# Kernel optimization log

Hardware: AMD Instinct MI355X
Metric: run time of the kernel (lower is better)

## Reference

```python
import jax, jax.numpy as jnp
import numpy as np

N_NODES = 100000
EMB_DIM = 64
N_EDGES = 1200000
N_LAYERS = 3


def setup_inputs() -> dict:
    key = jax.random.key(0)
    k1, k2, k3 = jax.random.split(key, 3)
    embedding = jax.random.normal(k1, (N_NODES, EMB_DIM), dtype=jnp.float32)
    layer_weights = jnp.ones((N_LAYERS + 1,), dtype=jnp.float32) / (N_LAYERS + 1)
    edge_weight = jax.random.uniform(k2, (N_EDGES,), dtype=jnp.float32)
    edge_index = jax.random.randint(k3, (2, N_EDGES), 0, N_NODES, dtype=jnp.int64)
    return {"embedding": embedding, "layer_weights": layer_weights,
            "edge_weight": edge_weight, "edge_index": edge_index}


def reference(embedding, layer_weights, edge_weight, edge_index):
    # LightGCN inference (dropout off). Each LGConv applies gcn_norm
    # (no self loops) then scatter-adds norm * x[src] into dst.
    n = embedding.shape[0]
    row, col = edge_index[0], edge_index[1]  # source, target

    # gcn_norm: deg over target nodes, symmetric normalization
    deg = jax.ops.segment_sum(edge_weight, col, num_segments=n)
    dinv = jnp.where(deg > 0, jax.lax.rsqrt(deg), 0.0)
    norm = dinv[row] * edge_weight * dinv[col]  # [E]

    x = embedding
    outs = [x]
    for _ in range(N_LAYERS):
        msgs = norm[:, None] * x[row]                         # [E, D] gather
        x = jax.ops.segment_sum(msgs, col, num_segments=n)    # [N, D] scatter
        outs.append(x)

    w = jax.nn.softmax(layer_weights)                         # [L+1]
    comb = jnp.einsum('l,lnd->nd', w, jnp.stack(outs))        # weighted layer combine
    # F.normalize(dim=1), eps=1e-12
    nrm = jnp.maximum(jnp.linalg.norm(comb, axis=1, keepdims=True), 1e-12)
    return comb / nrm
```

## Files before the change

kernel.cpp:

```cpp
#include <hip/hip_runtime.h>

#define N_NODES 100000
#define EMB_DIM 64
#define N_EDGES 1200000

#define BSHIFT  7
#define BNODES  128
#define NBUCKET ((N_NODES + BNODES - 1) / BNODES)
#define CAP     2048
#define EPB     4096
#define NBLK_BIN ((N_EDGES + EPB - 1) / EPB)

#define DBINS 512
#define DNPB  1024
#define NBLK_DEG ((N_NODES + DNPB - 1) / DNPB)

struct __align__(8) EdgeRec {
    int   s;
    float w;
};

struct __align__(8) BinRec {
    unsigned meta;
    float    ew;
};

__device__ __forceinline__ unsigned short f2bf(float f) {
    unsigned u = __float_as_uint(f);
    u += 0x7FFFu + ((u >> 16) & 1u);
    return (unsigned short)(u >> 16);
}
__device__ __forceinline__ float bf2f(unsigned short h) {
    return __uint_as_float((unsigned)h << 16);
}

__global__ void init_kernel(int* __restrict__ bucket_cursor, int* __restrict__ dhist) {
    int t = threadIdx.x;
    if (t < NBUCKET) bucket_cursor[t] = t * CAP;
    if (t < DBINS)   dhist[t] = 0;
}

__global__ void bin_scatter(const int* __restrict__ row,
                            const int* __restrict__ col,
                            const float* __restrict__ ew,
                            int* __restrict__ bucket_cursor,
                            BinRec* __restrict__ binned) {
    __shared__ int hcnt[NBUCKET];
    __shared__ int hbase[NBUCKET];
    int tid = threadIdx.x;
    if (tid < NBUCKET) hcnt[tid] = 0;
    __syncthreads();
    int base = blockIdx.x * EPB;
    int end = base + EPB; if (end > N_EDGES) end = N_EDGES;
    for (int e = base + tid; e < end; e += 1024)
        atomicAdd(&hcnt[col[e] >> BSHIFT], 1);
    __syncthreads();
    if (tid < NBUCKET) {
        int c = hcnt[tid];
        hbase[tid] = c ? atomicAdd(&bucket_cursor[tid], c) : 0;
        hcnt[tid] = 0;
    }
    __syncthreads();
    for (int e = base + tid; e < end; e += 1024) {
        int c = col[e];
        int b = c >> BSHIFT;
        int rk = atomicAdd(&hcnt[b], 1);
        BinRec r;
        r.meta = (unsigned)row[e] | ((unsigned)(c & (BNODES - 1)) << 20);
        r.ew = ew[e];
        binned[hbase[b] + rk] = r;
    }
}

__global__ void bucket_scan(const int* __restrict__ cursor,
                            int* __restrict__ csr_base,
                            int* __restrict__ start) {
    __shared__ int ws[16];
    int t = threadIdx.x;
    int lane = t & 63, wid = t >> 6;
    int v = (t < NBUCKET) ? (cursor[t] - t * CAP) : 0;
    int inc = v;
    #pragma unroll
    for (int o = 1; o < 64; o <<= 1) {
        int u = __shfl_up(inc, o, 64);
        if (lane >= o) inc += u;
    }
    if (lane == 63) ws[wid] = inc;
    __syncthreads();
    int woff = 0;
    for (int w = 0; w < wid; ++w) woff += ws[w];
    if (t < NBUCKET) csr_base[t] = woff + inc - v;
    if (t == 0) start[N_NODES] = N_EDGES;
}

__global__ void bucket_build(const BinRec* __restrict__ binned,
                             const int* __restrict__ cursor,
                             const int* __restrict__ csr_base,
                             float* __restrict__ dinv,
                             float* __restrict__ rdinv,
                             int* __restrict__ start,
                             EdgeRec* __restrict__ rec) {
    __shared__ int   cnt[BNODES];
    __shared__ float deg[BNODES];
    __shared__ int   cur[BNODES];
    __shared__ int   wsum[2];
    int b = blockIdx.x;
    int tid = threadIdx.x;
    if (tid < BNODES) { cnt[tid] = 0; deg[tid] = 0.0f; }
    __syncthreads();
    int s = b * CAP;
    int n = cursor[b] - s;
    for (int i = tid; i < n; i += 256) {
        BinRec r = binned[s + i];
        int l = r.meta >> 20;
        atomicAdd(&cnt[l], 1);
        atomicAdd(&deg[l], r.ew);
    }
    __syncthreads();
    int lane = tid & 63, wid = tid >> 6;
    int v = (tid < BNODES) ? cnt[tid] : 0;
    int inc = v;
    #pragma unroll
    for (int o = 1; o < 64; o <<= 1) {
        int u = __shfl_up(inc, o, 64);
        if (lane >= o) inc += u;
    }
    if (tid < BNODES && lane == 63) wsum[wid] = inc;
    __syncthreads();
    if (tid < BNODES) {
        int excl = inc - v + ((wid == 1) ? wsum[0] : 0);
        int node = (b << BSHIFT) + tid;
        if (node < N_NODES) {
            int st = csr_base[b] + excl;
            start[node] = st;
            cur[tid] = st;
            float d = deg[tid];
            dinv[node]  = (d > 0.0f) ? rsqrtf(d) : 0.0f;
            rdinv[node] = (d > 0.0f) ? sqrtf(d)  : 0.0f;
        } else {
            cur[tid] = 0;
        }
    }
    __syncthreads();
    for (int i = tid; i < n; i += 256) {
        BinRec r = binned[s + i];
        int l = r.meta >> 20;
        int pos = atomicAdd(&cur[l], 1);
        EdgeRec o;
        o.s = (int)(r.meta & 0xFFFFFu);
        o.w = r.ew;
        rec[pos] = o;
    }
}

__global__ void cvt_y0(const float* __restrict__ emb,
                       const float* __restrict__ dinv,
                       unsigned short* __restrict__ y0) {
    int t = blockIdx.x * blockDim.x + threadIdx.x;
    long base = (long)t * 8;
    if (base + 8 <= (long)N_NODES * EMB_DIM) {
        float dn = dinv[t >> 3];
        float4 a = *(const float4*)(emb + base);
        float4 b = *(const float4*)(emb + base + 4);
        uint4 o;
        o.x = (unsigned)f2bf(dn * a.x) | ((unsigned)f2bf(dn * a.y) << 16);
        o.y = (unsigned)f2bf(dn * a.z) | ((unsigned)f2bf(dn * a.w) << 16);
        o.z = (unsigned)f2bf(dn * b.x) | ((unsigned)f2bf(dn * b.y) << 16);
        o.w = (unsigned)f2bf(dn * b.z) | ((unsigned)f2bf(dn * b.w) << 16);
        *(uint4*)(y0 + base) = o;
    }
}

__global__ void deg_hist(const int* __restrict__ start, int* __restrict__ dhist) {
    __shared__ int h[DBINS];
    int tid = threadIdx.x;
    for (int i = tid; i < DBINS; i += 256) h[i] = 0;
    __syncthreads();
    int base = blockIdx.x * DNPB;
    int end = base + DNPB; if (end > N_NODES) end = N_NODES;
    for (int n = base + tid; n < end; n += 256) {
        int d = start[n + 1] - start[n];
        if (d > DBINS - 1) d = DBINS - 1;
        atomicAdd(&h[d], 1);
    }
    __syncthreads();
    for (int i = tid; i < DBINS; i += 256)
        if (h[i]) atomicAdd(&dhist[i], h[i]);
}

__global__ void deg_scan(const int* __restrict__ dhist, int* __restrict__ dcursor) {
    __shared__ int ws[8];
    int t = threadIdx.x;
    int lane = t & 63, wid = t >> 6;
    int v = dhist[t];
    int inc = v;
    #pragma unroll
    for (int o = 1; o < 64; o <<= 1) {
        int u = __shfl_up(inc, o, 64);
        if (lane >= o) inc += u;
    }
    if (lane == 63) ws[wid] = inc;
    __syncthreads();
    int woff = 0;
    for (int w = 0; w < wid; ++w) woff += ws[w];
    dcursor[t] = woff + inc - v;
}

__global__ void deg_scatter(const int* __restrict__ start,
                            int* __restrict__ dcursor,
                            int* __restrict__ perm) {
    __shared__ int h[DBINS];
    __shared__ int hb[DBINS];
    int tid = threadIdx.x;
    for (int i = tid; i < DBINS; i += 256) h[i] = 0;
    __syncthreads();
    int base = blockIdx.x * DNPB;
    int end = base + DNPB; if (end > N_NODES) end = N_NODES;
    for (int n = base + tid; n < end; n += 256) {
        int d = start[n + 1] - start[n];
        if (d > DBINS - 1) d = DBINS - 1;
        atomicAdd(&h[d], 1);
    }
    __syncthreads();
    for (int i = tid; i < DBINS; i += 256) {
        int c = h[i];
        hb[i] = c ? atomicAdd(&dcursor[i], c) : 0;
        h[i] = 0;
    }
    __syncthreads();
    for (int n = base + tid; n < end; n += 256) {
        int d = start[n + 1] - start[n];
        if (d > DBINS - 1) d = DBINS - 1;
        int rk = atomicAdd(&h[d], 1);
        perm[hb[d] + rk] = n;
    }
}

__global__ void prop16_kernel(const unsigned short* __restrict__ yin,
                              unsigned short* __restrict__ yout,
                              const EdgeRec* __restrict__ rec,
                              const int* __restrict__ start,
                              const float* __restrict__ dinv,
                              const int* __restrict__ perm) {
    int t = blockIdx.x * blockDim.x + threadIdx.x;
    int slot = t >> 4;
    int q = (t & 15) << 2;
    if (slot >= N_NODES) return;
    int n = perm[slot];
    int s = start[n], e = start[n + 1];
    float a0 = 0.f, a1 = 0.f, a2 = 0.f, a3 = 0.f;
    int j = s;
    for (; j + 2 <= e; j += 2) {
        EdgeRec r0 = rec[j], r1 = rec[j + 1];
        ushort4 h0 = *(const ushort4*)(yin + (((size_t)r0.s) << 6) + q);
        ushort4 h1 = *(const ushort4*)(yin + (((size_t)r1.s) << 6) + q);
        a0 += r0.w * bf2f(h0.x) + r1.w * bf2f(h1.x);
        a1 += r0.w * bf2f(h0.y) + r1.w * bf2f(h1.y);
        a2 += r0.w * bf2f(h0.z) + r1.w * bf2f(h1.z);
        a3 += r0.w * bf2f(h0.w) + r1.w * bf2f(h1.w);
    }
    if (j < e) {
        EdgeRec r = rec[j];
        ushort4 h = *(const ushort4*)(yin + (((size_t)r.s) << 6) + q);
        a0 += r.w * bf2f(h.x);
        a1 += r.w * bf2f(h.y);
        a2 += r.w * bf2f(h.z);
        a3 += r.w * bf2f(h.w);
    }
    float dn = dinv[n];
    float dn2 = dn * dn;
    ushort4 o;
    o.x = f2bf(dn2 * a0);
    o.y = f2bf(dn2 * a1);
    o.z = f2bf(dn2 * a2);
    o.w = f2bf(dn2 * a3);
    *(ushort4*)(yout + (((size_t)n) << 6) + q) = o;
}

__global__ void prop16_combine_kernel(const unsigned short* __restrict__ y2h,
                                      const float* __restrict__ x0,
                                      const unsigned short* __restrict__ y1h,
                                      const EdgeRec* __restrict__ rec,
                                      const int* __restrict__ start,
                                      const float* __restrict__ dinv,
                                      const float* __restrict__ rdinv,
                                      const float* __restrict__ lw,
                                      const int* __restrict__ perm,
                                      float* __restrict__ out) {
    int t = blockIdx.x * blockDim.x + threadIdx.x;
    int slot = t >> 4;
    int q = (t & 15) << 2;
    if (slot >= N_NODES) return;
    int n = perm[slot];
    int s = start[n], e = start[n + 1];
    float a0 = 0.f, a1 = 0.f, a2 = 0.f, a3 = 0.f;
    int j = s;
    for (; j + 2 <= e; j += 2) {
        EdgeRec r0 = rec[j], r1 = rec[j + 1];
        ushort4 h0 = *(const ushort4*)(y2h + (((size_t)r0.s) << 6) + q);
        ushort4 h1 = *(const ushort4*)(y2h + (((size_t)r1.s) << 6) + q);
        a0 += r0.w * bf2f(h0.x) + r1.w * bf2f(h1.x);
        a1 += r0.w * bf2f(h0.y) + r1.w * bf2f(h1.y);
        a2 += r0.w * bf2f(h0.z) + r1.w * bf2f(h1.z);
        a3 += r0.w * bf2f(h0.w) + r1.w * bf2f(h1.w);
    }
    if (j < e) {
        EdgeRec r = rec[j];
        ushort4 h = *(const ushort4*)(y2h + (((size_t)r.s) << 6) + q);
        a0 += r.w * bf2f(h.x);
        a1 += r.w * bf2f(h.y);
        a2 += r.w * bf2f(h.z);
        a3 += r.w * bf2f(h.w);
    }
    float dn = dinv[n];
    float rn = rdinv[n];
    float x3v0 = dn * a0, x3v1 = dn * a1, x3v2 = dn * a2, x3v3 = dn * a3;

    float w0 = lw[0], w1 = lw[1], w2 = lw[2], w3 = lw[3];
    float m = fmaxf(fmaxf(w0, w1), fmaxf(w2, w3));
    float e0 = expf(w0 - m), e1 = expf(w1 - m), e2 = expf(w2 - m), e3 = expf(w3 - m);
    float inv_s = 1.0f / (e0 + e1 + e2 + e3);

    size_t off = (((size_t)n) << 6) + q;
    float4 xv = *(const float4*)(x0 + off);
    ushort4 h1v = *(const ushort4*)(y1h + off);
    ushort4 h2v = *(const ushort4*)(y2h + off);

    float v0 = (e0 * xv.x + e1 * bf2f(h1v.x) * rn + e2 * bf2f(h2v.x) * rn + e3 * x3v0) * inv_s;
    float v1 = (e0 * xv.y + e1 * bf2f(h1v.y) * rn + e2 * bf2f(h2v.y) * rn + e3 * x3v1) * inv_s;
    float v2 = (e0 * xv.z + e1 * bf2f(h1v.z) * rn + e2 * bf2f(h2v.z) * rn + e3 * x3v2) * inv_s;
    float v3 = (e0 * xv.w + e1 * bf2f(h1v.w) * rn + e2 * bf2f(h2v.w) * rn + e3 * x3v3) * inv_s;

    float sq = v0 * v0 + v1 * v1 + v2 * v2 + v3 * v3;
    #pragma unroll
    for (int o = 1; o < 16; o <<= 1) sq += __shfl_xor(sq, o, 64);
    float nrm = fmaxf(sqrtf(sq), 1e-12f);
    float inv_n = 1.0f / nrm;

    float4 ov;
    ov.x = v0 * inv_n; ov.y = v1 * inv_n; ov.z = v2 * inv_n; ov.w = v3 * inv_n;
    *(float4*)(out + off) = ov;
}

extern "C" void kernel_launch(void* const* d_in, const int* in_sizes, int n_in,
                              void* d_out, int out_size, void* d_ws, size_t ws_size,
                              hipStream_t stream) {
    const float* emb = (const float*)d_in[0];
    const float* lw  = (const float*)d_in[1];
    const float* ew  = (const float*)d_in[2];
    const int*   ei  = (const int*)d_in[3];
    const int* row = ei;
    const int* col = ei + N_EDGES;
    float* out = (float*)d_out;

    char* p = (char*)d_ws;
    BinRec*  binned = (BinRec*)p;               p += (size_t)NBUCKET * CAP * sizeof(BinRec);
    EdgeRec* rec    = (EdgeRec*)p;              p += (size_t)N_EDGES * sizeof(EdgeRec);
    unsigned short* y0h = (unsigned short*)p;   p += (size_t)N_NODES * EMB_DIM * 2;
    unsigned short* y1h = (unsigned short*)p;   p += (size_t)N_NODES * EMB_DIM * 2;
    unsigned short* y2h = (unsigned short*)p;   p += (size_t)N_NODES * EMB_DIM * 2;
    float* dinv  = (float*)p;                   p += (size_t)N_NODES * 4;
    float* rdinv = (float*)p;                   p += (size_t)N_NODES * 4;
    int*   startA= (int*)p;                     p += (size_t)(N_NODES + 8) * 4;
    int*   perm  = (int*)p;                     p += (size_t)N_NODES * 4;
    int*   csr_base      = (int*)p;             p += (size_t)NBUCKET * 4;
    int*   bucket_cursor = (int*)p;             p += (size_t)NBUCKET * 4;
    int*   dhist   = (int*)p;                   p += (size_t)DBINS * 4;
    int*   dcursor = (int*)p;                   p += (size_t)DBINS * 4;

    const int B = 256;

    init_kernel<<<1, 1024, 0, stream>>>(bucket_cursor, dhist);
    bin_scatter<<<NBLK_BIN, 1024, 0, stream>>>(row, col, ew, bucket_cursor, binned);
    bucket_scan<<<1, 1024, 0, stream>>>(bucket_cursor, csr_base, startA);
    bucket_build<<<NBUCKET, B, 0, stream>>>(binned, bucket_cursor, csr_base,
                                            dinv, rdinv, startA, rec);
    cvt_y0<<<(N_NODES * EMB_DIM / 8 + B - 1) / B, B, 0, stream>>>(emb, dinv, y0h);
    deg_hist<<<NBLK_DEG, B, 0, stream>>>(startA, dhist);
    deg_scan<<<1, DBINS, 0, stream>>>(dhist, dcursor);
    deg_scatter<<<NBLK_DEG, B, 0, stream>>>(startA, dcursor, perm);

    long pt = (long)N_NODES * 16;
    int pgrid = (int)((pt + B - 1) / B);
    prop16_kernel<<<pgrid, B, 0, stream>>>(y0h, y1h, rec, startA, dinv, perm);
    prop16_kernel<<<pgrid, B, 0, stream>>>(y1h, y2h, rec, startA, dinv, perm);
    prop16_combine_kernel<<<pgrid, B, 0, stream>>>(y2h, emb, y1h, rec, startA, dinv,
                                                   rdinv, lw, perm, out);
}
```

Measured before the change: 168.9 us.

## Fuse y0 conversion and degree histogram into bucket_build; widen propagation to 8 lanes per node

Folds the bf16 y0 conversion and the degree histogram into bucket_build, which removes two kernel launches and a reread of start/dinv. The propagation and combine kernels now use 8 threads per node, each loading 16-byte bf16 vectors, with the edge loop unrolled by 4. This gives more memory-level parallelism per thread and fewer threads in total. The cost is higher register pressure and lower occupancy, and the average degree of 12 per node limits how much the 4-way unroll helps.

```diff
diff --git a/kernel.cpp b/kernel.cpp
--- a/kernel.cpp
+++ b/kernel.cpp
@@ -14,6 +14,8 @@
 #define DBINS 512
 #define DNPB  1024
 #define NBLK_DEG ((N_NODES + DNPB - 1) / DNPB)
+
+typedef unsigned short ushort8v __attribute__((ext_vector_type(8)));
 
 struct __align__(8) EdgeRec {
     int   s;
@@ -96,17 +98,22 @@
 __global__ void bucket_build(const BinRec* __restrict__ binned,
                              const int* __restrict__ cursor,
                              const int* __restrict__ csr_base,
+                             const float* __restrict__ emb,
                              float* __restrict__ dinv,
                              float* __restrict__ rdinv,
                              int* __restrict__ start,
-                             EdgeRec* __restrict__ rec) {
+                             EdgeRec* __restrict__ rec,
+                             unsigned short* __restrict__ y0,
+                             int* __restrict__ dhist) {
     __shared__ int   cnt[BNODES];
     __shared__ float deg[BNODES];
     __shared__ int   cur[BNODES];
+    __shared__ int   dh[DBINS];
     __shared__ int   wsum[2];
     int b = blockIdx.x;
     int tid = threadIdx.x;
     if (tid < BNODES) { cnt[tid] = 0; deg[tid] = 0.0f; }
+    for (int i = tid; i < DBINS; i += 256) dh[i] = 0;
     __syncthreads();
     int s = b * CAP;
     int n = cursor[b] - s;
@@ -137,6 +144,8 @@
             float d = deg[tid];
             dinv[node]  = (d > 0.0f) ? rsqrtf(d) : 0.0f;
             rdinv[node] = (d > 0.0f) ? sqrtf(d)  : 0.0f;
+            int dd = v; if (dd > DBINS - 1) dd = DBINS - 1;
+            atomicAdd(&dh[dd], 1);
         } else {
             cur[tid] = 0;
         }
@@ -151,41 +160,27 @@
         o.w = r.ew;
         rec[pos] = o;
     }
-}
-
-__global__ void cvt_y0(const float* __restrict__ emb,
-                       const float* __restrict__ dinv,
-                       unsigned short* __restrict__ y0) {
-    int t = blockIdx.x * blockDim.x + threadIdx.x;
-    long base = (long)t * 8;
-    if (base + 8 <= (long)N_NODES * EMB_DIM) {
-        float dn = dinv[t >> 3];
-        float4 a = *(const float4*)(emb + base);
-        float4 b = *(const float4*)(emb + base + 4);
-        uint4 o;
-        o.x = (unsigned)f2bf(dn * a.x) | ((unsigned)f2bf(dn * a.y) << 16);
-        o.y = (unsigned)f2bf(dn * a.z) | ((unsigned)f2bf(dn * a.w) << 16);
-        o.z = (unsigned)f2bf(dn * b.x) | ((unsigned)f2bf(dn * b.y) << 16);
-        o.w = (unsigned)f2bf(dn * b.z) | ((unsigned)f2bf(dn * b.w) << 16);
-        *(uint4*)(y0 + base) = o;
-    }
-}
-
-__global__ void deg_hist(const int* __restrict__ start, int* __restrict__ dhist) {
-    __shared__ int h[DBINS];
-    int tid = threadIdx.x;
-    for (int i = tid; i < DBINS; i += 256) h[i] = 0;
-    __syncthreads();
-    int base = blockIdx.x * DNPB;
-    int end = base + DNPB; if (end > N_NODES) end = N_NODES;
-    for (int n = base + tid; n < end; n += 256) {
-        int d = start[n + 1] - start[n];
-        if (d > DBINS - 1) d = DBINS - 1;
-        atomicAdd(&h[d], 1);
-    }
-    __syncthreads();
     for (int i = tid; i < DBINS; i += 256)
-        if (h[i]) atomicAdd(&dhist[i], h[i]);
+        if (dh[i]) atomicAdd(&dhist[i], dh[i]);
+    #pragma unroll
+    for (int pass = 0; pass < 4; ++pass) {
+        int g = (pass * 256 + tid) * 8;
+        int l = g >> 6;
+        int node = (b << BSHIFT) + l;
+        if (node < N_NODES) {
+            float d = deg[l];
+            float dn = (d > 0.0f) ? rsqrtf(d) : 0.0f;
+            size_t off = (((size_t)node) << 6) + (g & 63);
+            float4 a = *(const float4*)(emb + off);
+            float4 bb = *(const float4*)(emb + off + 4);
+            uint4 o;
+            o.x = (unsigned)f2bf(dn * a.x)  | ((unsigned)f2bf(dn * a.y)  << 16);
+            o.y = (unsigned)f2bf(dn * a.z)  | ((unsigned)f2bf(dn * a.w)  << 16);
+            o.z = (unsigned)f2bf(dn * bb.x) | ((unsigned)f2bf(dn * bb.y) << 16);
+            o.w = (unsigned)f2bf(dn * bb.z) | ((unsigned)f2bf(dn * bb.w) << 16);
+            *(uint4*)(y0 + off) = o;
+        }
+    }
 }
 
 __global__ void deg_scan(const int* __restrict__ dhist, int* __restrict__ dcursor) {
@@ -236,110 +231,131 @@
     }
 }
 
-__global__ void prop16_kernel(const unsigned short* __restrict__ yin,
-                              unsigned short* __restrict__ yout,
-                              const EdgeRec* __restrict__ rec,
-                              const int* __restrict__ start,
-                              const float* __restrict__ dinv,
-                              const int* __restrict__ perm) {
+__global__ void prop8_kernel(const unsigned short* __restrict__ yin,
+                             unsigned short* __restrict__ yout,
+                             const EdgeRec* __restrict__ rec,
+                             const int* __restrict__ start,
+                             const float* __restrict__ dinv,
+                             const int* __restrict__ perm) {
     int t = blockIdx.x * blockDim.x + threadIdx.x;
-    int slot = t >> 4;
-    int q = (t & 15) << 2;
+    int slot = t >> 3;
+    int q = (t & 7) << 3;
     if (slot >= N_NODES) return;
     int n = perm[slot];
     int s = start[n], e = start[n + 1];
     float a0 = 0.f, a1 = 0.f, a2 = 0.f, a3 = 0.f;
+    float a4 = 0.f, a5 = 0.f, a6 = 0.f, a7 = 0.f;
     int j = s;
-    for (; j + 2 <= e; j += 2) {
-        EdgeRec r0 = rec[j], r1 = rec[j + 1];
-        ushort4 h0 = *(const ushort4*)(yin + (((size_t)r0.s) << 6) + q);
-        ushort4 h1 = *(const ushort4*)(yin + (((size_t)r1.s) << 6) + q);
-        a0 += r0.w * bf2f(h0.x) + r1.w * bf2f(h1.x);
-        a1 += r0.w * bf2f(h0.y) + r1.w * bf2f(h1.y);
-        a2 += r0.w * bf2f(h0.z) + r1.w * bf2f(h1.z);
-        a3 += r0.w * bf2f(h0.w) + r1.w * bf2f(h1.w);
-    }
-    if (j < e) {
+    for (; j + 4 <= e; j += 4) {
+        EdgeRec r0 = rec[j], r1 = rec[j + 1], r2 = rec[j + 2], r3 = rec[j + 3];
+        ushort8v h0 = *(const ushort8v*)(yin + (((size_t)r0.s) << 6) + q);
+        ushort8v h1 = *(const ushort8v*)(yin + (((size_t)r1.s) << 6) + q);
+        ushort8v h2 = *(const ushort8v*)(yin + (((size_t)r2.s) << 6) + q);
+        ushort8v h3 = *(const ushort8v*)(yin + (((size_t)r3.s) << 6) + q);
+        a0 += r0.w * bf2f(h0[0]) + r1.w * bf2f(h1[0]) + r2.w * bf2f(h2[0]) + r3.w * bf2f(h3[0]);
+        a1 += r0.w * bf2f(h0[1]) + r1.w * bf2f(h1[1]) + r2.w * bf2f(h2[1]) + r3.w * bf2f(h3[1]);
+        a2 += r0.w * bf2f(h0[2]) + r1.w * bf2f(h1[2]) + r2.w * bf2f(h2[2]) + r3.w * bf2f(h3[2]);
+        a3 += r0.w * bf2f(h0[3]) + r1.w * bf2f(h1[3]) + r2.w * bf2f(h2[3]) + r3.w * bf2f(h3[3]);
+        a4 += r0.w * bf2f(h0[4]) + r1.w * bf2f(h1[4]) + r2.w * bf2f(h2[4]) + r3.w * bf2f(h3[4]);
+        a5 += r0.w * bf2f(h0[5]) + r1.w * bf2f(h1[5]) + r2.w * bf2f(h2[5]) + r3.w * bf2f(h3[5]);
+        a6 += r0.w * bf2f(h0[6]) + r1.w * bf2f(h1[6]) + r2.w * bf2f(h2[6]) + r3.w * bf2f(h3[6]);
+        a7 += r0.w * bf2f(h0[7]) + r1.w * bf2f(h1[7]) + r2.w * bf2f(h2[7]) + r3.w * bf2f(h3[7]);
+    }
+    for (; j < e; ++j) {
         EdgeRec r = rec[j];
-        ushort4 h = *(const ushort4*)(yin + (((size_t)r.s) << 6) + q);
-        a0 += r.w * bf2f(h.x);
-        a1 += r.w * bf2f(h.y);
-        a2 += r.w * bf2f(h.z);
-        a3 += r.w * bf2f(h.w);
+        ushort8v h = *(const ushort8v*)(yin + (((size_t)r.s) << 6) + q);
+        a0 += r.w * bf2f(h[0]); a1 += r.w * bf2f(h[1]);
+        a2 += r.w * bf2f(h[2]); a3 += r.w * bf2f(h[3]);
+        a4 += r.w * bf2f(h[4]); a5 += r.w * bf2f(h[5]);
+        a6 += r.w * bf2f(h[6]); a7 += r.w * bf2f(h[7]);
     }
     float dn = dinv[n];
     float dn2 = dn * dn;
-    ushort4 o;
-    o.x = f2bf(dn2 * a0);
-    o.y = f2bf(dn2 * a1);
-    o.z = f2bf(dn2 * a2);
-    o.w = f2bf(dn2 * a3);
-    *(ushort4*)(yout + (((size_t)n) << 6) + q) = o;
-}
-
-__global__ void prop16_combine_kernel(const unsigned short* __restrict__ y2h,
-                                      const float* __restrict__ x0,
-                                      const unsigned short* __restrict__ y1h,
-                                      const EdgeRec* __restrict__ rec,
-                                      const int* __restrict__ start,
-                                      const float* __restrict__ dinv,
-                                      const float* __restrict__ rdinv,
-                                      const float* __restrict__ lw,
-                                      const int* __restrict__ perm,
-                                      float* __restrict__ out) {
+    uint4 o;
+    o.x = (unsigned)f2bf(dn2 * a0) | ((unsigned)f2bf(dn2 * a1) << 16);
+    o.y = (unsigned)f2bf(dn2 * a2) | ((unsigned)f2bf(dn2 * a3) << 16);
+    o.z = (unsigned)f2bf(dn2 * a4) | ((unsigned)f2bf(dn2 * a5) << 16);
+    o.w = (unsigned)f2bf(dn2 * a6) | ((unsigned)f2bf(dn2 * a7) << 16);
+    *(uint4*)(yout + (((size_t)n) << 6) + q) = o;
+}
+
+__global__ void prop8_combine_kernel(const unsigned short* __restrict__ y2h,
+                                     const float* __restrict__ x0,
+                                     const unsigned short* __restrict__ y1h,
+                                     const EdgeRec* __restrict__ rec,
+                                     const int* __restrict__ start,
+                                     const float* __restrict__ dinv,
+                                     const float* __restrict__ rdinv,
+                                     const float* __restrict__ lw,
+                                     const int* __restrict__ perm,
+                                     float* __restrict__ out) {
     int t = blockIdx.x * blockDim.x + threadIdx.x;
-    int slot = t >> 4;
-    int q = (t & 15) << 2;
+    int slot = t >> 3;
+    int q = (t & 7) << 3;
     if (slot >= N_NODES) return;
     int n = perm[slot];
     int s = start[n], e = start[n + 1];
     float a0 = 0.f, a1 = 0.f, a2 = 0.f, a3 = 0.f;
+    float a4 = 0.f, a5 = 0.f, a6 = 0.f, a7 = 0.f;
     int j = s;
-    for (; j + 2 <= e; j += 2) {
-        EdgeRec r0 = rec[j], r1 = rec[j + 1];
-        ushort4 h0 = *(const ushort4*)(y2h + (((size_t)r0.s) << 6) + q);
-        ushort4 h1 = *(const ushort4*)(y2h + (((size_t)r1.s) << 6) + q);
-        a0 += r0.w * bf2f(h0.x) + r1.w * bf2f(h1.x);
-        a1 += r0.w * bf2f(h0.y) + r1.w * bf2f(h1.y);
-        a2 += r0.w * bf2f(h0.z) + r1.w * bf2f(h1.z);
-        a3 += r0.w * bf2f(h0.w) + r1.w * bf2f(h1.w);
-    }
-    if (j < e) {
+    for (; j + 4 <= e; j += 4) {
+        EdgeRec r0 = rec[j], r1 = rec[j + 1], r2 = rec[j + 2], r3 = rec[j + 3];
+        ushort8v h0 = *(const ushort8v*)(y2h + (((size_t)r0.s) << 6) + q);
+        ushort8v h1 = *(const ushort8v*)(y2h + (((size_t)r1.s) << 6) + q);
+        ushort8v h2 = *(const ushort8v*)(y2h + (((size_t)r2.s) << 6) + q);
+        ushort8v h3 = *(const ushort8v*)(y2h + (((size_t)r3.s) << 6) + q);
+        a0 += r0.w * bf2f(h0[0]) + r1.w * bf2f(h1[0]) + r2.w * bf2f(h2[0]) + r3.w * bf2f(h3[0]);
+        a1 += r0.w * bf2f(h0[1]) + r1.w * bf2f(h1[1]) + r2.w * bf2f(h2[1]) + r3.w * bf2f(h3[1]);
+        a2 += r0.w * bf2f(h0[2]) + r1.w * bf2f(h1[2]) + r2.w * bf2f(h2[2]) + r3.w * bf2f(h3[2]);
+        a3 += r0.w * bf2f(h0[3]) + r1.w * bf2f(h1[3]) + r2.w * bf2f(h2[3]) + r3.w * bf2f(h3[3]);
+        a4 += r0.w * bf2f(h0[4]) + r1.w * bf2f(h1[4]) + r2.w * bf2f(h2[4]) + r3.w * bf2f(h3[4]);
+        a5 += r0.w * bf2f(h0[5]) + r1.w * bf2f(h1[5]) + r2.w * bf2f(h2[5]) + r3.w * bf2f(h3[5]);
+        a6 += r0.w * bf2f(h0[6]) + r1.w * bf2f(h1[6]) + r2.w * bf2f(h2[6]) + r3.w * bf2f(h3[6]);
+        a7 += r0.w * bf2f(h0[7]) + r1.w * bf2f(h1[7]) + r2.w * bf2f(h2[7]) + r3.w * bf2f(h3[7]);
+    }
+    for (; j < e; ++j) {
         EdgeRec r = rec[j];
-        ushort4 h = *(const ushort4*)(y2h + (((size_t)r.s) << 6) + q);
-        a0 += r.w * bf2f(h.x);
-        a1 += r.w * bf2f(h.y);
-        a2 += r.w * bf2f(h.z);
-        a3 += r.w * bf2f(h.w);
+        ushort8v h = *(const ushort8v*)(y2h + (((size_t)r.s) << 6) + q);
+        a0 += r.w * bf2f(h[0]); a1 += r.w * bf2f(h[1]);
+        a2 += r.w * bf2f(h[2]); a3 += r.w * bf2f(h[3]);
+        a4 += r.w * bf2f(h[4]); a5 += r.w * bf2f(h[5]);
+        a6 += r.w * bf2f(h[6]); a7 += r.w * bf2f(h[7]);
     }
     float dn = dinv[n];
     float rn = rdinv[n];
-    float x3v0 = dn * a0, x3v1 = dn * a1, x3v2 = dn * a2, x3v3 = dn * a3;
 
     float w0 = lw[0], w1 = lw[1], w2 = lw[2], w3 = lw[3];
     float m = fmaxf(fmaxf(w0, w1), fmaxf(w2, w3));
     float e0 = expf(w0 - m), e1 = expf(w1 - m), e2 = expf(w2 - m), e3 = expf(w3 - m);
     float inv_s = 1.0f / (e0 + e1 + e2 + e3);
+    float c1 = e1 * rn, c2 = e2 * rn, c3 = e3 * dn;
 
     size_t off = (((size_t)n) << 6) + q;
-    float4 xv = *(const float4*)(x0 + off);
-    ushort4 h1v = *(const ushort4*)(y1h + off);
-    ushort4 h2v = *(const ushort4*)(y2h + off);
-
-    float v0 = (e0 * xv.x + e1 * bf2f(h1v.x) * rn + e2 * bf2f(h2v.x) * rn + e3 * x3v0) * inv_s;
-    float v1 = (e0 * xv.y + e1 * bf2f(h1v.y) * rn + e2 * bf2f(h2v.y) * rn + e3 * x3v1) * inv_s;
-    float v2 = (e0 * xv.z + e1 * bf2f(h1v.z) * rn + e2 * bf2f(h2v.z) * rn + e3 * x3v2) * inv_s;
-    float v3 = (e0 * xv.w + e1 * bf2f(h1v.w) * rn + e2 * bf2f(h2v.w) * rn + e3 * x3v3) * inv_s;
-
-    float sq = v0 * v0 + v1 * v1 + v2 * v2 + v3 * v3;
+    float4 xa = *(const float4*)(x0 + off);
+    float4 xb = *(const float4*)(x0 + off + 4);
+    ushort8v h1v = *(const ushort8v*)(y1h + off);
+    ushort8v h2v = *(const ushort8v*)(y2h + off);
+
+    float v0 = (e0 * xa.x + c1 * bf2f(h1v[0]) + c2 * bf2f(h2v[0]) + c3 * a0) * inv_s;
+    float v1 = (e0 * xa.y + c1 * bf2f(h1v[1]) + c2 * bf2f(h2v[1]) + c3 * a1) * inv_s;
+    float v2 = (e0 * xa.z + c1 * bf2f(h1v[2]) + c2 * bf2f(h2v[2]) + c3 * a2) * inv_s;
+    float v3 = (e0 * xa.w + c1 * bf2f(h1v[3]) + c2 * bf2f(h2v[3]) + c3 * a3) * inv_s;
+    float v4 = (e0 * xb.x + c1 * bf2f(h1v[4]) + c2 * bf2f(h2v[4]) + c3 * a4) * inv_s;
+    float v5 = (e0 * xb.y + c1 * bf2f(h1v[5]) + c2 * bf2f(h2v[5]) + c3 * a5) * inv_s;
+    float v6 = (e0 * xb.z + c1 * bf2f(h1v[6]) + c2 * bf2f(h2v[6]) + c3 * a6) * inv_s;
+    float v7 = (e0 * xb.w + c1 * bf2f(h1v[7]) + c2 * bf2f(h2v[7]) + c3 * a7) * inv_s;
+
+    float sq = v0*v0 + v1*v1 + v2*v2 + v3*v3 + v4*v4 + v5*v5 + v6*v6 + v7*v7;
     #pragma unroll
-    for (int o = 1; o < 16; o <<= 1) sq += __shfl_xor(sq, o, 64);
+    for (int o = 1; o < 8; o <<= 1) sq += __shfl_xor(sq, o, 64);
     float nrm = fmaxf(sqrtf(sq), 1e-12f);
     float inv_n = 1.0f / nrm;
 
-    float4 ov;
-    ov.x = v0 * inv_n; ov.y = v1 * inv_n; ov.z = v2 * inv_n; ov.w = v3 * inv_n;
-    *(float4*)(out + off) = ov;
+    float4 oa, ob;
+    oa.x = v0 * inv_n; oa.y = v1 * inv_n; oa.z = v2 * inv_n; oa.w = v3 * inv_n;
+    ob.x = v4 * inv_n; ob.y = v5 * inv_n; ob.z = v6 * inv_n; ob.w = v7 * inv_n;
+    *(float4*)(out + off) = oa;
+    *(float4*)(out + off + 4) = ob;
 }
 
 extern "C" void kernel_launch(void* const* d_in, const int* in_sizes, int n_in,
@@ -373,17 +389,15 @@
     init_kernel<<<1, 1024, 0, stream>>>(bucket_cursor, dhist);
     bin_scatter<<<NBLK_BIN, 1024, 0, stream>>>(row, col, ew, bucket_cursor, binned);
     bucket_scan<<<1, 1024, 0, stream>>>(bucket_cursor, csr_base, startA);
-    bucket_build<<<NBUCKET, B, 0, stream>>>(binned, bucket_cursor, csr_base,
-                                            dinv, rdinv, startA, rec);
-    cvt_y0<<<(N_NODES * EMB_DIM / 8 + B - 1) / B, B, 0, stream>>>(emb, dinv, y0h);
-    deg_hist<<<NBLK_DEG, B, 0, stream>>>(startA, dhist);
+    bucket_build<<<NBUCKET, B, 0, stream>>>(binned, bucket_cursor, csr_base, emb,
+                                            dinv, rdinv, startA, rec, y0h, dhist);
     deg_scan<<<1, DBINS, 0, stream>>>(dhist, dcursor);
     deg_scatter<<<NBLK_DEG, B, 0, stream>>>(startA, dcursor, perm);
 
-    long pt = (long)N_NODES * 16;
+    long pt = (long)N_NODES * 8;
     int pgrid = (int)((pt + B - 1) / B);
-    prop16_kernel<<<pgrid, B, 0, stream>>>(y0h, y1h, rec, startA, dinv, perm);
-    prop16_kernel<<<pgrid, B, 0, stream>>>(y1h, y2h, rec, startA, dinv, perm);
-    prop16_combine_kernel<<<pgrid, B, 0, stream>>>(y2h, emb, y1h, rec, startA, dinv,
-                                                   rdinv, lw, perm, out);
-}
+    prop8_kernel<<<pgrid, B, 0, stream>>>(y0h, y1h, rec, startA, dinv, perm);
+    prop8_kernel<<<pgrid, B, 0, stream>>>(y1h, y2h, rec, startA, dinv, perm);
+    prop8_combine_kernel<<<pgrid, B, 0, stream>>>(y2h, emb, y1h, rec, startA, dinv,
+                                                  rdinv, lw, perm, out);
+}
```

Result: faster. 157.1 us (-7.0%).
